# Performance work log

Measured on AMD Instinct MI355X. Metric: run time of the kernel, lower is better.

## Reference

```python
import jax, jax.numpy as jnp
import numpy as np

B, K, D = 16384, 64, 128


def setup_inputs() -> dict:
    key = jax.random.key(0)
    kx, kc = jax.random.split(key)
    x = jax.random.normal(kx, (B, D), dtype=jnp.float32)
    centers = jax.random.uniform(kc, (K, D), dtype=jnp.float32)  # torch.rand init
    return {"x": x, "centers": centers}


def reference(x, centers):
    batch, dim = x.shape
    k = centers.shape[0]
    # pairwise squared distances, same math as sum((x - c)^2)
    diff = x[:, None, :] - centers[None, :, :]          # [B, K, D]
    dist_sq = jnp.sum(diff * diff, axis=-1)             # [B, K]
    expo = -0.5 * dist_sq
    # safe softmax over clusters (identical to max-subtracted exp/sum)
    resp = jax.nn.softmax(expo, axis=-1)                # [B, K]
    log_resp = jnp.log(jnp.clip(resp, 1e-8))
    # hard assignment and per-cluster statistics
    assign = jnp.argmin(dist_sq, axis=-1)               # [B] int
    onehot = jax.nn.one_hot(assign, k, dtype=x.dtype)   # [B, K]
    cluster_weight = jnp.sum(onehot, axis=0)            # [K]
    emp_total = jnp.einsum('nk,nd->kd', onehot, x)      # [K, D]
    emp_mean = emp_total / (cluster_weight[:, None] + 1e-7)
    # masked centered samples: onehot[n,k]*(x_n - mean_k) is nonzero only at k=assign(n)
    xm = x - emp_mean[assign]                           # [B, D]
    covar_total = jnp.einsum('nk,nd,ne->kde', onehot, xm, xm)  # [K, D, D]
    covar = covar_total / (cluster_weight[:, None, None] + 1e-7)
    eye = jnp.eye(dim, dtype=x.dtype)
    covar_diag = covar * eye
    covar_off = covar * (1.0 - eye)
    diag_dist_sq = jnp.sum((covar_diag - eye) ** 2, axis=(1, 2))  # [K]
    off_dist_sq = jnp.sum(covar_off ** 2, axis=(1, 2))            # [K]
    mean_dist_sq = jnp.sum((emp_mean - centers) ** 2, axis=1)     # [K]
    mean_mse = jnp.sum(cluster_weight * mean_dist_sq) / (batch * dim)
    covar_mse = jnp.sum(
        cluster_weight * diag_dist_sq / (batch * dim)
        + cluster_weight * off_dist_sq / (batch * dim * (dim - 1.0))
    )
    return log_resp, mean_mse, covar_mse
```

## Files before the change

### kernel.cpp

```cpp
#include <hip/hip_runtime.h>

#define BB 16384
#define KK 64
#define DD 128
#define SEG 128
#define MAXITEMS 256
#define RSLAB 2048

typedef __attribute__((ext_vector_type(8))) short bf16x8;
typedef __attribute__((ext_vector_type(4))) float f32x4;

__device__ __forceinline__ unsigned int packbf2(float a, float b) {
    unsigned ua = __float_as_uint(a);
    unsigned ub = __float_as_uint(b);
    ua = (ua + 0x7FFFu + ((ua >> 16) & 1u)) >> 16;
    ub = (ub + 0x7FFFu + ((ub >> 16) & 1u)) >> 16;
    return ua | (ub << 16);
}

__global__ __launch_bounds__(256) void k_rows(
    const float* __restrict__ x, const float* __restrict__ centers,
    float* __restrict__ log_resp, int* __restrict__ assign,
    int* __restrict__ bhist, float* __restrict__ outscalars,
    float* __restrict__ emp)
{
    __shared__ float xs[64][132];
    __shared__ float ct[DD][66];
    __shared__ float cn2[KK];
    __shared__ int   lh[KK];

    const int tid = threadIdx.x;
    const int row0 = blockIdx.x * 64;

    if (blockIdx.x == 0 && tid < 2) outscalars[tid] = 0.f;
    if (tid < 32) emp[blockIdx.x * 32 + tid] = 0.f;
    if (tid < KK) lh[tid] = 0;

    for (int g = tid; g < 64 * 32; g += 256) {
        int r = g >> 5, c4 = g & 31;
        float4 v = ((const float4*)(x + (size_t)(row0 + r) * DD))[c4];
        *(float4*)&xs[r][c4 * 4] = v;
    }
    for (int g = tid; g < KK * 32; g += 256) {
        int k = g >> 5, c4 = g & 31;
        float4 v = ((const float4*)(centers + (size_t)k * DD))[c4];
        ct[c4 * 4 + 0][k] = v.x;
        ct[c4 * 4 + 1][k] = v.y;
        ct[c4 * 4 + 2][k] = v.z;
        ct[c4 * 4 + 3][k] = v.w;
    }
    __syncthreads();
    if (tid < KK) {
        float s = 0.f;
        for (int d = 0; d < DD; ++d) { float c = ct[d][tid]; s = fmaf(c, c, s); }
        cn2[tid] = s;
    }
    __syncthreads();

    const int tr = tid >> 5;
    const int tc = tid & 31;
    const int k0 = tc * 2, k1 = k0 + 1;

    float acc0[8], acc1[8];
    #pragma unroll
    for (int i = 0; i < 8; ++i) { acc0[i] = 0.f; acc1[i] = 0.f; }

    for (int d = 0; d < DD; d += 4) {
        float2 b0 = *(const float2*)&ct[d + 0][k0];
        float2 b1 = *(const float2*)&ct[d + 1][k0];
        float2 b2 = *(const float2*)&ct[d + 2][k0];
        float2 b3 = *(const float2*)&ct[d + 3][k0];
        #pragma unroll
        for (int i = 0; i < 8; ++i) {
            float4 a = *(const float4*)&xs[tr * 8 + i][d];
            acc0[i] = fmaf(a.x, b0.x, acc0[i]);
            acc1[i] = fmaf(a.x, b0.y, acc1[i]);
            acc0[i] = fmaf(a.y, b1.x, acc0[i]);
            acc1[i] = fmaf(a.y, b1.y, acc1[i]);
            acc0[i] = fmaf(a.z, b2.x, acc0[i]);
            acc1[i] = fmaf(a.z, b2.y, acc1[i]);
            acc0[i] = fmaf(a.w, b3.x, acc0[i]);
            acc1[i] = fmaf(a.w, b3.y, acc1[i]);
        }
    }

    const float cn0 = 0.5f * cn2[k0], cn1 = 0.5f * cn2[k1];
    #pragma unroll
    for (int i = 0; i < 8; ++i) {
        int row = row0 + tr * 8 + i;
        float v0 = acc0[i] - cn0;
        float v1 = acc1[i] - cn1;
        float m; int idx;
        if (v1 > v0) { m = v1; idx = k1; } else { m = v0; idx = k0; }
        #pragma unroll
        for (int off = 1; off < 32; off <<= 1) {
            float ov = __shfl_xor(m, off);
            int   oi = __shfl_xor(idx, off);
            if (ov > m || (ov == m && oi < idx)) { m = ov; idx = oi; }
        }
        float s = expf(v0 - m) + expf(v1 - m);
        #pragma unroll
        for (int off = 1; off < 32; off <<= 1) s += __shfl_xor(s, off);
        float ls = logf(s);
        float lr0 = fmaxf(v0 - m - ls, -18.4206807f);
        float lr1 = fmaxf(v1 - m - ls, -18.4206807f);
        *(float2*)&log_resp[(size_t)row * KK + k0] = make_float2(lr0, lr1);
        if (tc == 0) {
            assign[row] = idx;
            atomicAdd(&lh[idx], 1);
        }
    }
    __syncthreads();
    if (tid < KK) bhist[blockIdx.x * KK + tid] = lh[tid];
}

__global__ __launch_bounds__(256) void k_scat(
    const int* __restrict__ assign, const int* __restrict__ bhist,
    int* __restrict__ sorted, float* __restrict__ cw,
    int4* __restrict__ items, int* __restrict__ item_count,
    int* __restrict__ ist, int* __restrict__ ien)
{
    __shared__ int ph_tot[4][KK], ph_pre[4][KK];
    __shared__ int cnt_s[KK], pre_s[KK], base_s[KK], cur_s[KK];

    const int tid = threadIdx.x;
    const int b = blockIdx.x;
    const int t = tid & 63, q = tid >> 6;

    int tot = 0, pre = 0;
    const int bb0 = q * 64;
    for (int bb = bb0; bb < bb0 + 64; ++bb) {
        int v = bhist[bb * KK + t];
        tot += v;
        if (bb < b) pre += v;
    }
    ph_tot[q][t] = tot; ph_pre[q][t] = pre;
    __syncthreads();

    if (tid < KK) {
        cnt_s[tid] = ph_tot[0][tid] + ph_tot[1][tid] + ph_tot[2][tid] + ph_tot[3][tid];
        pre_s[tid] = ph_pre[0][tid] + ph_pre[1][tid] + ph_pre[2][tid] + ph_pre[3][tid];
        cur_s[tid] = 0;
    }
    __syncthreads();
    if (tid == 0) {
        int base = 0;
        for (int k = 0; k < KK; ++k) { base_s[k] = base; base += cnt_s[k]; }
    }
    __syncthreads();

    if (tid < 64) {
        int r = b * 64 + tid;
        int a = assign[r];
        int p = base_s[a] + pre_s[a] + atomicAdd(&cur_s[a], 1);
        sorted[p] = r;
    }

    if (b == 0) {
        if (tid < KK) cw[tid] = (float)cnt_s[tid];
        if (tid == 0) {
            int ic = 0;
            for (int k = 0; k < KK; ++k) {
                ist[k] = ic;
                int c = cnt_s[k];
                for (int s = 0; s < c; s += SEG) {
                    int4 it; it.x = k; it.y = base_s[k] + s;
                    it.z = min(SEG, c - s); it.w = 0;
                    items[ic++] = it;
                }
                ien[k] = ic;
            }
            *item_count = ic;
        }
    }
}

__global__ __launch_bounds__(256) void k_seg(
    const float* __restrict__ x, const int* __restrict__ sorted,
    const int4* __restrict__ items, const int* __restrict__ item_count,
    float* __restrict__ part, float* __restrict__ emp)
{
    if ((int)blockIdx.x >= *item_count) return;
    int4 it = items[blockIdx.x];
    const int k = it.x, gstart = it.y, len = it.z;

    __shared__ int rows_s[SEG];
    __shared__ unsigned int XT[DD][68];

    const int tid = threadIdx.x;
    const int w = tid >> 6, lane = tid & 63;

    if (tid < len) rows_s[tid] = sorted[gstart + tid];
    __syncthreads();

    {
        const int r0 = 2 * lane, r1 = 2 * lane + 1;
        const int d0 = w * 32;
        const float* p0 = x + (size_t)rows_s[r0 < len ? r0 : 0] * DD + d0;
        const float* p1 = x + (size_t)rows_s[r1 < len ? r1 : 0] * DD + d0;
        #pragma unroll
        for (int i = 0; i < 8; ++i) {
            float4 a = make_float4(0.f, 0.f, 0.f, 0.f);
            float4 b = make_float4(0.f, 0.f, 0.f, 0.f);
            if (r0 < len) a = *(const float4*)(p0 + 4 * i);
            if (r1 < len) b = *(const float4*)(p1 + 4 * i);
            XT[d0 + 4 * i + 0][lane] = packbf2(a.x, b.x);
            XT[d0 + 4 * i + 1][lane] = packbf2(a.y, b.y);
            XT[d0 + 4 * i + 2][lane] = packbf2(a.z, b.z);
            XT[d0 + 4 * i + 3][lane] = packbf2(a.w, b.w);
        }
    }
    __syncthreads();

    if (tid < DD) {
        float s = 0.f;
        #pragma unroll
        for (int j4 = 0; j4 < 16; ++j4) {
            uint4 v = *(const uint4*)&XT[tid][j4 * 4];
            s += __uint_as_float(v.x << 16) + __uint_as_float(v.x & 0xFFFF0000u);
            s += __uint_as_float(v.y << 16) + __uint_as_float(v.y & 0xFFFF0000u);
            s += __uint_as_float(v.z << 16) + __uint_as_float(v.z & 0xFFFF0000u);
            s += __uint_as_float(v.w << 16) + __uint_as_float(v.w & 0xFFFF0000u);
        }
        atomicAdd(&emp[k * DD + tid], s);
    }

    const int c4 = lane & 15, q = lane >> 4;
    f32x4 acc[2][8];
    #pragma unroll
    for (int h = 0; h < 2; ++h)
        #pragma unroll
        for (int nt = 0; nt < 8; ++nt)
            acc[h][nt] = (f32x4){0.f, 0.f, 0.f, 0.f};

    #pragma unroll
    for (int c = 0; c < 4; ++c) {
        const int ku = c * 16 + q * 4;
        bf16x8 a0 = *(const bf16x8*)&XT[(2 * w + 0) * 16 + c4][ku];
        bf16x8 a1 = *(const bf16x8*)&XT[(2 * w + 1) * 16 + c4][ku];
        #pragma unroll
        for (int nt = 0; nt < 8; ++nt) {
            bf16x8 b = *(const bf16x8*)&XT[nt * 16 + c4][ku];
            acc[0][nt] = __builtin_amdgcn_mfma_f32_16x16x32_bf16(a0, b, acc[0][nt], 0, 0, 0);
            acc[1][nt] = __builtin_amdgcn_mfma_f32_16x16x32_bf16(a1, b, acc[1][nt], 0, 0, 0);
        }
    }

    float* pb = part + (size_t)blockIdx.x * (DD * DD);
    #pragma unroll
    for (int h = 0; h < 2; ++h) {
        const int m0 = (2 * w + h) * 16 + q * 4;
        #pragma unroll
        for (int nt = 0; nt < 8; ++nt) {
            const int n = nt * 16 + c4;
            pb[(m0 + 0) * DD + n] = acc[h][nt].x;
            pb[(m0 + 1) * DD + n] = acc[h][nt].y;
            pb[(m0 + 2) * DD + n] = acc[h][nt].z;
            pb[(m0 + 3) * DD + n] = acc[h][nt].w;
        }
    }
}

__global__ __launch_bounds__(256) void k_redfinal(
    const float* __restrict__ part, const float* __restrict__ emp,
    const float* __restrict__ cw, const float* __restrict__ centers,
    const int* __restrict__ ist, const int* __restrict__ ien,
    float* __restrict__ outscalars)
{
    const int k = blockIdx.x >> 3;
    const int p = blockIdx.x & 7;
    const int i0 = ist[k], i1 = ien[k];
    const int tid = threadIdx.x;
    const int w = tid >> 6, lane = tid & 63;
    const float wgt = cw[k];
    const float inv = 1.0f / (wgt + 1e-7f);

    __shared__ float mu_s[DD], emp_s[DD];
    __shared__ float red[4][RSLAB];

    if (tid < DD) {
        float e = emp[k * DD + tid];
        emp_s[tid] = e;
        mu_s[tid] = e * inv;
    }

    float4 acc[8];
    #pragma unroll
    for (int c = 0; c < 8; ++c) acc[c] = make_float4(0.f, 0.f, 0.f, 0.f);

    const int base = p * RSLAB;
    for (int it = i0 + w; it < i1; it += 4) {
        const float* pb = part + (size_t)it * (DD * DD) + base;
        #pragma unroll
        for (int c = 0; c < 8; ++c) {
            float4 v = *(const float4*)&pb[c * 256 + lane * 4];
            acc[c].x += v.x; acc[c].y += v.y; acc[c].z += v.z; acc[c].w += v.w;
        }
    }
    #pragma unroll
    for (int c = 0; c < 8; ++c)
        *(float4*)&red[w][c * 256 + lane * 4] = acc[c];
    __syncthreads();

    float ds = 0.f, os = 0.f, mm = 0.f;
    #pragma unroll
    for (int jj = 0; jj < 8; ++jj) {
        int el = jj * 256 + tid;
        float sx = red[0][el] + red[1][el] + red[2][el] + red[3][el];
        int gel = base + el;
        int d = gel >> 7, e = gel & 127;
        float ctv = sx - mu_s[d] * emp_s[e] - emp_s[d] * mu_s[e]
                  + wgt * mu_s[d] * mu_s[e];
        float v = ctv * inv;
        if (d == e) { float t = v - 1.f; ds += t * t; }
        else        { os += v * v; }
    }
    if (p == 0 && tid < DD) {
        float t = mu_s[tid] - centers[k * DD + tid];
        mm = t * t;
    }

    #pragma unroll
    for (int off = 32; off > 0; off >>= 1) {
        ds += __shfl_down(ds, off);
        os += __shfl_down(os, off);
        mm += __shfl_down(mm, off);
    }
    __shared__ float rds[4], ros[4], rmm[4];
    if (lane == 0) { rds[w] = ds; ros[w] = os; rmm[w] = mm; }
    __syncthreads();
    if (tid == 0) {
        float DS = rds[0] + rds[1] + rds[2] + rds[3];
        float OS = ros[0] + ros[1] + ros[2] + ros[3];
        float MM = rmm[0] + rmm[1] + rmm[2] + rmm[3];
        const float bd = (float)BB * (float)DD;
        atomicAdd(&outscalars[0], wgt * MM / bd);
        atomicAdd(&outscalars[1], wgt * DS / bd + wgt * OS / (bd * (float)(DD - 1)));
    }
}

extern "C" void kernel_launch(void* const* d_in, const int* in_sizes, int n_in,
                              void* d_out, int out_size, void* d_ws, size_t ws_size,
                              hipStream_t stream) {
    const float* x = (const float*)d_in[0];
    const float* centers = (const float*)d_in[1];
    float* out = (float*)d_out;
    float* outscalars = out + (size_t)BB * KK;

    char* ws = (char*)d_ws;
    size_t off = 0;
    float* part    = (float*)(ws + off); off += (size_t)MAXITEMS * DD * DD * 4;
    float* emp     = (float*)(ws + off); off += KK * DD * 4;
    int*   sorted  = (int*)  (ws + off); off += BB * 4;
    int*   assign  = (int*)  (ws + off); off += BB * 4;
    int*   bhist   = (int*)  (ws + off); off += 256 * KK * 4;
    int4*  items   = (int4*) (ws + off); off += MAXITEMS * 16;
    float* cw      = (float*)(ws + off); off += 256;
    int*   itemcnt = (int*)  (ws + off); off += 256;
    int*   ist     = (int*)  (ws + off); off += 256;
    int*   ien     = (int*)  (ws + off); off += 256;

    k_rows    <<<256, 256, 0, stream>>>(x, centers, out, assign, bhist,
                                        outscalars, emp);
    k_scat    <<<256, 256, 0, stream>>>(assign, bhist, sorted, cw, items,
                                        itemcnt, ist, ien);
    k_seg     <<<MAXITEMS, 256, 0, stream>>>(x, sorted, items, itemcnt, part, emp);
    k_redfinal<<<KK * 8, 256, 0, stream>>>(part, emp, cw, centers, ist, ien,
                                           outscalars);
}
```

Measured before the change: 128.3 us.

## Double segment length per block and spread partial reduction across more blocks

Each k_seg block now handles up to 256 rows of its cluster in two 128-row halves, keeping MFMA accumulators in registers across both halves. That halves the number of 128x128 partial covariance slabs written to and re-read from global memory. The final reduction now uses 64 blocks per cluster with one element per thread and no shared-memory staging, giving more parallelism. k_seg launches only 128 blocks, so there is less parallelism there, and the halves run serially within each block.

```diff
diff --git a/kernel.cpp b/kernel.cpp
--- a/kernel.cpp
+++ b/kernel.cpp
@@ -3,9 +3,9 @@
 #define BB 16384
 #define KK 64
 #define DD 128
-#define SEG 128
+#define SEG 256
 #define MAXITEMS 256
-#define RSLAB 2048
+#define NS 64
 
 typedef __attribute__((ext_vector_type(8))) short bf16x8;
 typedef __attribute__((ext_vector_type(4))) float f32x4;
@@ -184,67 +184,77 @@
     int4 it = items[blockIdx.x];
     const int k = it.x, gstart = it.y, len = it.z;
 
-    __shared__ int rows_s[SEG];
+    __shared__ int rows_s[128];
     __shared__ unsigned int XT[DD][68];
 
     const int tid = threadIdx.x;
     const int w = tid >> 6, lane = tid & 63;
-
-    if (tid < len) rows_s[tid] = sorted[gstart + tid];
-    __syncthreads();
-
-    {
-        const int r0 = 2 * lane, r1 = 2 * lane + 1;
-        const int d0 = w * 32;
-        const float* p0 = x + (size_t)rows_s[r0 < len ? r0 : 0] * DD + d0;
-        const float* p1 = x + (size_t)rows_s[r1 < len ? r1 : 0] * DD + d0;
-        #pragma unroll
-        for (int i = 0; i < 8; ++i) {
-            float4 a = make_float4(0.f, 0.f, 0.f, 0.f);
-            float4 b = make_float4(0.f, 0.f, 0.f, 0.f);
-            if (r0 < len) a = *(const float4*)(p0 + 4 * i);
-            if (r1 < len) b = *(const float4*)(p1 + 4 * i);
-            XT[d0 + 4 * i + 0][lane] = packbf2(a.x, b.x);
-            XT[d0 + 4 * i + 1][lane] = packbf2(a.y, b.y);
-            XT[d0 + 4 * i + 2][lane] = packbf2(a.z, b.z);
-            XT[d0 + 4 * i + 3][lane] = packbf2(a.w, b.w);
-        }
-    }
-    __syncthreads();
-
-    if (tid < DD) {
-        float s = 0.f;
-        #pragma unroll
-        for (int j4 = 0; j4 < 16; ++j4) {
-            uint4 v = *(const uint4*)&XT[tid][j4 * 4];
-            s += __uint_as_float(v.x << 16) + __uint_as_float(v.x & 0xFFFF0000u);
-            s += __uint_as_float(v.y << 16) + __uint_as_float(v.y & 0xFFFF0000u);
-            s += __uint_as_float(v.z << 16) + __uint_as_float(v.z & 0xFFFF0000u);
-            s += __uint_as_float(v.w << 16) + __uint_as_float(v.w & 0xFFFF0000u);
-        }
-        atomicAdd(&emp[k * DD + tid], s);
-    }
-
     const int c4 = lane & 15, q = lane >> 4;
+
     f32x4 acc[2][8];
     #pragma unroll
     for (int h = 0; h < 2; ++h)
         #pragma unroll
         for (int nt = 0; nt < 8; ++nt)
             acc[h][nt] = (f32x4){0.f, 0.f, 0.f, 0.f};
-
-    #pragma unroll
-    for (int c = 0; c < 4; ++c) {
-        const int ku = c * 16 + q * 4;
-        bf16x8 a0 = *(const bf16x8*)&XT[(2 * w + 0) * 16 + c4][ku];
-        bf16x8 a1 = *(const bf16x8*)&XT[(2 * w + 1) * 16 + c4][ku];
-        #pragma unroll
-        for (int nt = 0; nt < 8; ++nt) {
-            bf16x8 b = *(const bf16x8*)&XT[nt * 16 + c4][ku];
-            acc[0][nt] = __builtin_amdgcn_mfma_f32_16x16x32_bf16(a0, b, acc[0][nt], 0, 0, 0);
-            acc[1][nt] = __builtin_amdgcn_mfma_f32_16x16x32_bf16(a1, b, acc[1][nt], 0, 0, 0);
-        }
-    }
+    float colsum = 0.f;
+
+    for (int half = 0; half < 2; ++half) {
+        const int hoff = half * 128;
+        const int hlen = min(128, len - hoff);
+        if (hlen <= 0) break;
+
+        __syncthreads();
+        if (tid < hlen) rows_s[tid] = sorted[gstart + hoff + tid];
+        __syncthreads();
+
+        {
+            const int r0 = 2 * lane, r1 = 2 * lane + 1;
+            const int d0 = w * 32;
+            const float* p0 = x + (size_t)rows_s[r0 < hlen ? r0 : 0] * DD + d0;
+            const float* p1 = x + (size_t)rows_s[r1 < hlen ? r1 : 0] * DD + d0;
+            #pragma unroll
+            for (int i = 0; i < 8; ++i) {
+                float4 a = make_float4(0.f, 0.f, 0.f, 0.f);
+                float4 b = make_float4(0.f, 0.f, 0.f, 0.f);
+                if (r0 < hlen) a = *(const float4*)(p0 + 4 * i);
+                if (r1 < hlen) b = *(const float4*)(p1 + 4 * i);
+                XT[d0 + 4 * i + 0][lane] = packbf2(a.x, b.x);
+                XT[d0 + 4 * i + 1][lane] = packbf2(a.y, b.y);
+                XT[d0 + 4 * i + 2][lane] = packbf2(a.z, b.z);
+                XT[d0 + 4 * i + 3][lane] = packbf2(a.w, b.w);
+            }
+        }
+        __syncthreads();
+
+        if (tid < DD) {
+            float s = 0.f;
+            #pragma unroll
+            for (int j4 = 0; j4 < 16; ++j4) {
+                uint4 v = *(const uint4*)&XT[tid][j4 * 4];
+                s += __uint_as_float(v.x << 16) + __uint_as_float(v.x & 0xFFFF0000u);
+                s += __uint_as_float(v.y << 16) + __uint_as_float(v.y & 0xFFFF0000u);
+                s += __uint_as_float(v.z << 16) + __uint_as_float(v.z & 0xFFFF0000u);
+                s += __uint_as_float(v.w << 16) + __uint_as_float(v.w & 0xFFFF0000u);
+            }
+            colsum += s;
+        }
+
+        #pragma unroll
+        for (int c = 0; c < 4; ++c) {
+            const int ku = c * 16 + q * 4;
+            bf16x8 a0 = *(const bf16x8*)&XT[(2 * w + 0) * 16 + c4][ku];
+            bf16x8 a1 = *(const bf16x8*)&XT[(2 * w + 1) * 16 + c4][ku];
+            #pragma unroll
+            for (int nt = 0; nt < 8; ++nt) {
+                bf16x8 b = *(const bf16x8*)&XT[nt * 16 + c4][ku];
+                acc[0][nt] = __builtin_amdgcn_mfma_f32_16x16x32_bf16(a0, b, acc[0][nt], 0, 0, 0);
+                acc[1][nt] = __builtin_amdgcn_mfma_f32_16x16x32_bf16(a1, b, acc[1][nt], 0, 0, 0);
+            }
+        }
+    }
+
+    if (tid < DD) atomicAdd(&emp[k * DD + tid], colsum);
 
     float* pb = part + (size_t)blockIdx.x * (DD * DD);
     #pragma unroll
@@ -267,8 +277,8 @@
     const int* __restrict__ ist, const int* __restrict__ ien,
     float* __restrict__ outscalars)
 {
-    const int k = blockIdx.x >> 3;
-    const int p = blockIdx.x & 7;
+    const int k = blockIdx.x >> 6;
+    const int p = blockIdx.x & (NS - 1);
     const int i0 = ist[k], i1 = ien[k];
     const int tid = threadIdx.x;
     const int w = tid >> 6, lane = tid & 63;
@@ -276,45 +286,30 @@
     const float inv = 1.0f / (wgt + 1e-7f);
 
     __shared__ float mu_s[DD], emp_s[DD];
-    __shared__ float red[4][RSLAB];
-
     if (tid < DD) {
         float e = emp[k * DD + tid];
         emp_s[tid] = e;
         mu_s[tid] = e * inv;
     }
-
-    float4 acc[8];
-    #pragma unroll
-    for (int c = 0; c < 8; ++c) acc[c] = make_float4(0.f, 0.f, 0.f, 0.f);
-
-    const int base = p * RSLAB;
-    for (int it = i0 + w; it < i1; it += 4) {
-        const float* pb = part + (size_t)it * (DD * DD) + base;
-        #pragma unroll
-        for (int c = 0; c < 8; ++c) {
-            float4 v = *(const float4*)&pb[c * 256 + lane * 4];
-            acc[c].x += v.x; acc[c].y += v.y; acc[c].z += v.z; acc[c].w += v.w;
-        }
-    }
-    #pragma unroll
-    for (int c = 0; c < 8; ++c)
-        *(float4*)&red[w][c * 256 + lane * 4] = acc[c];
-    __syncthreads();
-
+    __syncthreads();
+
+    const int gel = p * 256 + tid;
+    float s0 = 0.f, s1 = 0.f;
+    int it = i0;
+    for (; it + 1 < i1; it += 2) {
+        s0 += part[(size_t)it * (DD * DD) + gel];
+        s1 += part[(size_t)(it + 1) * (DD * DD) + gel];
+    }
+    if (it < i1) s0 += part[(size_t)it * (DD * DD) + gel];
+    const float sx = s0 + s1;
+
+    const int d = gel >> 7, e = gel & 127;
+    float ctv = sx - mu_s[d] * emp_s[e] - emp_s[d] * mu_s[e]
+              + wgt * mu_s[d] * mu_s[e];
+    float v = ctv * inv;
     float ds = 0.f, os = 0.f, mm = 0.f;
-    #pragma unroll
-    for (int jj = 0; jj < 8; ++jj) {
-        int el = jj * 256 + tid;
-        float sx = red[0][el] + red[1][el] + red[2][el] + red[3][el];
-        int gel = base + el;
-        int d = gel >> 7, e = gel & 127;
-        float ctv = sx - mu_s[d] * emp_s[e] - emp_s[d] * mu_s[e]
-                  + wgt * mu_s[d] * mu_s[e];
-        float v = ctv * inv;
-        if (d == e) { float t = v - 1.f; ds += t * t; }
-        else        { os += v * v; }
-    }
+    if (d == e) { float t = v - 1.f; ds = t * t; }
+    else        { os = v * v; }
     if (p == 0 && tid < DD) {
         float t = mu_s[tid] - centers[k * DD + tid];
         mm = t * t;
@@ -364,7 +359,7 @@
                                         outscalars, emp);
     k_scat    <<<256, 256, 0, stream>>>(assign, bhist, sorted, cw, items,
                                         itemcnt, ist, ien);
-    k_seg     <<<MAXITEMS, 256, 0, stream>>>(x, sorted, items, itemcnt, part, emp);
-    k_redfinal<<<KK * 8, 256, 0, stream>>>(part, emp, cw, centers, ist, ien,
-                                           outscalars);
-}
+    k_seg     <<<128, 256, 0, stream>>>(x, sorted, items, itemcnt, part, emp);
+    k_redfinal<<<KK * NS, 256, 0, stream>>>(part, emp, cw, centers, ist, ien,
+                                            outscalars);
+}
```

After: 220.4 us. 71.7% more time.

## Double segment length, replace atomics with per-item partials and last-block reduce

Applied to the files above, without the earlier changes.

Each k_seg block now handles up to 256 rows in two 128-row halves and accumulates into the same MFMA registers. That halves the number of 128x128 partial covariance matrices written to and re-read from global memory. The per-cluster column-sum atomics are replaced by per-item partial vectors, which k_redfinal sums itself. The final scalar atomics become a counter-based last-block reduction over per-block results. In exchange, k_redfinal uses a 64 KB shared slab per block, which lowers occupancy, and k_seg has more serial work per block.

```diff
diff --git a/kernel.cpp b/kernel.cpp
--- a/kernel.cpp
+++ b/kernel.cpp
@@ -3,9 +3,11 @@
 #define BB 16384
 #define KK 64
 #define DD 128
-#define SEG 128
-#define MAXITEMS 256
-#define RSLAB 2048
+#define SEG 256
+#define MAXITEMS 128
+#define NRB 4
+#define RSLAB 4096
+#define RBLKS (KK * NRB)
 
 typedef __attribute__((ext_vector_type(8))) short bf16x8;
 typedef __attribute__((ext_vector_type(4))) float f32x4;
@@ -21,8 +23,7 @@
 __global__ __launch_bounds__(256) void k_rows(
     const float* __restrict__ x, const float* __restrict__ centers,
     float* __restrict__ log_resp, int* __restrict__ assign,
-    int* __restrict__ bhist, float* __restrict__ outscalars,
-    float* __restrict__ emp)
+    int* __restrict__ bhist, int* __restrict__ counter)
 {
     __shared__ float xs[64][132];
     __shared__ float ct[DD][66];
@@ -32,8 +33,7 @@
     const int tid = threadIdx.x;
     const int row0 = blockIdx.x * 64;
 
-    if (blockIdx.x == 0 && tid < 2) outscalars[tid] = 0.f;
-    if (tid < 32) emp[blockIdx.x * 32 + tid] = 0.f;
+    if (blockIdx.x == 0 && tid == 0) *counter = 0;
     if (tid < KK) lh[tid] = 0;
 
     for (int g = tid; g < 64 * 32; g += 256) {
@@ -178,73 +178,83 @@
 __global__ __launch_bounds__(256) void k_seg(
     const float* __restrict__ x, const int* __restrict__ sorted,
     const int4* __restrict__ items, const int* __restrict__ item_count,
-    float* __restrict__ part, float* __restrict__ emp)
+    float* __restrict__ part, float* __restrict__ emp_part)
 {
     if ((int)blockIdx.x >= *item_count) return;
     int4 it = items[blockIdx.x];
-    const int k = it.x, gstart = it.y, len = it.z;
-
-    __shared__ int rows_s[SEG];
+    const int gstart = it.y, len = it.z;
+
+    __shared__ int rows_s[128];
     __shared__ unsigned int XT[DD][68];
 
     const int tid = threadIdx.x;
     const int w = tid >> 6, lane = tid & 63;
-
-    if (tid < len) rows_s[tid] = sorted[gstart + tid];
-    __syncthreads();
-
-    {
-        const int r0 = 2 * lane, r1 = 2 * lane + 1;
-        const int d0 = w * 32;
-        const float* p0 = x + (size_t)rows_s[r0 < len ? r0 : 0] * DD + d0;
-        const float* p1 = x + (size_t)rows_s[r1 < len ? r1 : 0] * DD + d0;
-        #pragma unroll
-        for (int i = 0; i < 8; ++i) {
-            float4 a = make_float4(0.f, 0.f, 0.f, 0.f);
-            float4 b = make_float4(0.f, 0.f, 0.f, 0.f);
-            if (r0 < len) a = *(const float4*)(p0 + 4 * i);
-            if (r1 < len) b = *(const float4*)(p1 + 4 * i);
-            XT[d0 + 4 * i + 0][lane] = packbf2(a.x, b.x);
-            XT[d0 + 4 * i + 1][lane] = packbf2(a.y, b.y);
-            XT[d0 + 4 * i + 2][lane] = packbf2(a.z, b.z);
-            XT[d0 + 4 * i + 3][lane] = packbf2(a.w, b.w);
-        }
-    }
-    __syncthreads();
-
-    if (tid < DD) {
-        float s = 0.f;
-        #pragma unroll
-        for (int j4 = 0; j4 < 16; ++j4) {
-            uint4 v = *(const uint4*)&XT[tid][j4 * 4];
-            s += __uint_as_float(v.x << 16) + __uint_as_float(v.x & 0xFFFF0000u);
-            s += __uint_as_float(v.y << 16) + __uint_as_float(v.y & 0xFFFF0000u);
-            s += __uint_as_float(v.z << 16) + __uint_as_float(v.z & 0xFFFF0000u);
-            s += __uint_as_float(v.w << 16) + __uint_as_float(v.w & 0xFFFF0000u);
-        }
-        atomicAdd(&emp[k * DD + tid], s);
-    }
-
     const int c4 = lane & 15, q = lane >> 4;
+
     f32x4 acc[2][8];
     #pragma unroll
     for (int h = 0; h < 2; ++h)
         #pragma unroll
         for (int nt = 0; nt < 8; ++nt)
             acc[h][nt] = (f32x4){0.f, 0.f, 0.f, 0.f};
-
-    #pragma unroll
-    for (int c = 0; c < 4; ++c) {
-        const int ku = c * 16 + q * 4;
-        bf16x8 a0 = *(const bf16x8*)&XT[(2 * w + 0) * 16 + c4][ku];
-        bf16x8 a1 = *(const bf16x8*)&XT[(2 * w + 1) * 16 + c4][ku];
-        #pragma unroll
-        for (int nt = 0; nt < 8; ++nt) {
-            bf16x8 b = *(const bf16x8*)&XT[nt * 16 + c4][ku];
-            acc[0][nt] = __builtin_amdgcn_mfma_f32_16x16x32_bf16(a0, b, acc[0][nt], 0, 0, 0);
-            acc[1][nt] = __builtin_amdgcn_mfma_f32_16x16x32_bf16(a1, b, acc[1][nt], 0, 0, 0);
-        }
-    }
+    float colsum = 0.f;
+
+    for (int half = 0; half < 2; ++half) {
+        const int hoff = half * 128;
+        const int hlen = min(128, len - hoff);
+        if (hlen <= 0) break;
+
+        __syncthreads();
+        if (tid < hlen) rows_s[tid] = sorted[gstart + hoff + tid];
+        __syncthreads();
+
+        {
+            const int r0 = 2 * lane, r1 = 2 * lane + 1;
+            const int d0 = w * 32;
+            const float* p0 = x + (size_t)rows_s[r0 < hlen ? r0 : 0] * DD + d0;
+            const float* p1 = x + (size_t)rows_s[r1 < hlen ? r1 : 0] * DD + d0;
+            #pragma unroll
+            for (int i = 0; i < 8; ++i) {
+                float4 a = make_float4(0.f, 0.f, 0.f, 0.f);
+                float4 b = make_float4(0.f, 0.f, 0.f, 0.f);
+                if (r0 < hlen) a = *(const float4*)(p0 + 4 * i);
+                if (r1 < hlen) b = *(const float4*)(p1 + 4 * i);
+                XT[d0 + 4 * i + 0][lane] = packbf2(a.x, b.x);
+                XT[d0 + 4 * i + 1][lane] = packbf2(a.y, b.y);
+                XT[d0 + 4 * i + 2][lane] = packbf2(a.z, b.z);
+                XT[d0 + 4 * i + 3][lane] = packbf2(a.w, b.w);
+            }
+        }
+        __syncthreads();
+
+        if (tid < DD) {
+            float s = 0.f;
+            #pragma unroll
+            for (int j4 = 0; j4 < 16; ++j4) {
+                uint4 v = *(const uint4*)&XT[tid][j4 * 4];
+                s += __uint_as_float(v.x << 16) + __uint_as_float(v.x & 0xFFFF0000u);
+                s += __uint_as_float(v.y << 16) + __uint_as_float(v.y & 0xFFFF0000u);
+                s += __uint_as_float(v.z << 16) + __uint_as_float(v.z & 0xFFFF0000u);
+                s += __uint_as_float(v.w << 16) + __uint_as_float(v.w & 0xFFFF0000u);
+            }
+            colsum += s;
+        }
+
+        #pragma unroll
+        for (int c = 0; c < 4; ++c) {
+            const int ku = c * 16 + q * 4;
+            bf16x8 a0 = *(const bf16x8*)&XT[(2 * w + 0) * 16 + c4][ku];
+            bf16x8 a1 = *(const bf16x8*)&XT[(2 * w + 1) * 16 + c4][ku];
+            #pragma unroll
+            for (int nt = 0; nt < 8; ++nt) {
+                bf16x8 b = *(const bf16x8*)&XT[nt * 16 + c4][ku];
+                acc[0][nt] = __builtin_amdgcn_mfma_f32_16x16x32_bf16(a0, b, acc[0][nt], 0, 0, 0);
+                acc[1][nt] = __builtin_amdgcn_mfma_f32_16x16x32_bf16(a1, b, acc[1][nt], 0, 0, 0);
+            }
+        }
+    }
+
+    if (tid < DD) emp_part[blockIdx.x * DD + tid] = colsum;
 
     float* pb = part + (size_t)blockIdx.x * (DD * DD);
     #pragma unroll
@@ -262,13 +272,14 @@
 }
 
 __global__ __launch_bounds__(256) void k_redfinal(
-    const float* __restrict__ part, const float* __restrict__ emp,
+    const float* __restrict__ part, const float* __restrict__ emp_part,
     const float* __restrict__ cw, const float* __restrict__ centers,
     const int* __restrict__ ist, const int* __restrict__ ien,
+    float2* __restrict__ spart, int* __restrict__ counter,
     float* __restrict__ outscalars)
 {
-    const int k = blockIdx.x >> 3;
-    const int p = blockIdx.x & 7;
+    const int k = blockIdx.x >> 2;
+    const int p = blockIdx.x & 3;
     const int i0 = ist[k], i1 = ien[k];
     const int tid = threadIdx.x;
     const int w = tid >> 6, lane = tid & 63;
@@ -276,35 +287,48 @@
     const float inv = 1.0f / (wgt + 1e-7f);
 
     __shared__ float mu_s[DD], emp_s[DD];
+    __shared__ float emp2[2][DD];
     __shared__ float red[4][RSLAB];
 
+    {
+        const int dh = tid & 127, hf = tid >> 7;
+        float e0 = 0.f, e1 = 0.f;
+        int it = i0 + hf;
+        for (; it + 2 < i1; it += 4) {
+            e0 += emp_part[it * DD + dh];
+            e1 += emp_part[(it + 2) * DD + dh];
+        }
+        if (it < i1) e0 += emp_part[it * DD + dh];
+        emp2[hf][dh] = e0 + e1;
+    }
+    __syncthreads();
     if (tid < DD) {
-        float e = emp[k * DD + tid];
+        float e = emp2[0][tid] + emp2[1][tid];
         emp_s[tid] = e;
         mu_s[tid] = e * inv;
     }
 
-    float4 acc[8];
-    #pragma unroll
-    for (int c = 0; c < 8; ++c) acc[c] = make_float4(0.f, 0.f, 0.f, 0.f);
+    float4 acc[16];
+    #pragma unroll
+    for (int c = 0; c < 16; ++c) acc[c] = make_float4(0.f, 0.f, 0.f, 0.f);
 
     const int base = p * RSLAB;
     for (int it = i0 + w; it < i1; it += 4) {
         const float* pb = part + (size_t)it * (DD * DD) + base;
         #pragma unroll
-        for (int c = 0; c < 8; ++c) {
+        for (int c = 0; c < 16; ++c) {
             float4 v = *(const float4*)&pb[c * 256 + lane * 4];
             acc[c].x += v.x; acc[c].y += v.y; acc[c].z += v.z; acc[c].w += v.w;
         }
     }
     #pragma unroll
-    for (int c = 0; c < 8; ++c)
+    for (int c = 0; c < 16; ++c)
         *(float4*)&red[w][c * 256 + lane * 4] = acc[c];
     __syncthreads();
 
     float ds = 0.f, os = 0.f, mm = 0.f;
     #pragma unroll
-    for (int jj = 0; jj < 8; ++jj) {
+    for (int jj = 0; jj < 16; ++jj) {
         int el = jj * 256 + tid;
         float sx = red[0][el] + red[1][el] + red[2][el] + red[3][el];
         int gel = base + el;
@@ -327,6 +351,7 @@
         mm += __shfl_down(mm, off);
     }
     __shared__ float rds[4], ros[4], rmm[4];
+    __shared__ int is_last;
     if (lane == 0) { rds[w] = ds; ros[w] = os; rmm[w] = mm; }
     __syncthreads();
     if (tid == 0) {
@@ -334,8 +359,31 @@
         float OS = ros[0] + ros[1] + ros[2] + ros[3];
         float MM = rmm[0] + rmm[1] + rmm[2] + rmm[3];
         const float bd = (float)BB * (float)DD;
-        atomicAdd(&outscalars[0], wgt * MM / bd);
-        atomicAdd(&outscalars[1], wgt * DS / bd + wgt * OS / (bd * (float)(DD - 1)));
+        float2 mine;
+        mine.x = wgt * MM / bd;
+        mine.y = wgt * DS / bd + wgt * OS / (bd * (float)(DD - 1));
+        spart[blockIdx.x] = mine;
+        __threadfence();
+        int old = atomicAdd(counter, 1);
+        is_last = (old == RBLKS - 1);
+    }
+    __syncthreads();
+    if (is_last) {
+        __threadfence();
+        float2 v = (tid < RBLKS) ? spart[tid] : make_float2(0.f, 0.f);
+        float a = v.x, b = v.y;
+        #pragma unroll
+        for (int off = 32; off > 0; off >>= 1) {
+            a += __shfl_down(a, off);
+            b += __shfl_down(b, off);
+        }
+        __shared__ float ra[4], rb[4];
+        if (lane == 0) { ra[w] = a; rb[w] = b; }
+        __syncthreads();
+        if (tid == 0) {
+            outscalars[0] = ra[0] + ra[1] + ra[2] + ra[3];
+            outscalars[1] = rb[0] + rb[1] + rb[2] + rb[3];
+        }
     }
 }
 
@@ -349,22 +397,24 @@
 
     char* ws = (char*)d_ws;
     size_t off = 0;
-    float* part    = (float*)(ws + off); off += (size_t)MAXITEMS * DD * DD * 4;
-    float* emp     = (float*)(ws + off); off += KK * DD * 4;
-    int*   sorted  = (int*)  (ws + off); off += BB * 4;
-    int*   assign  = (int*)  (ws + off); off += BB * 4;
-    int*   bhist   = (int*)  (ws + off); off += 256 * KK * 4;
-    int4*  items   = (int4*) (ws + off); off += MAXITEMS * 16;
-    float* cw      = (float*)(ws + off); off += 256;
-    int*   itemcnt = (int*)  (ws + off); off += 256;
-    int*   ist     = (int*)  (ws + off); off += 256;
-    int*   ien     = (int*)  (ws + off); off += 256;
-
-    k_rows    <<<256, 256, 0, stream>>>(x, centers, out, assign, bhist,
-                                        outscalars, emp);
+    float*  part     = (float*)(ws + off); off += (size_t)MAXITEMS * DD * DD * 4;
+    float*  emp_part = (float*)(ws + off); off += MAXITEMS * DD * 4;
+    int*    sorted   = (int*)  (ws + off); off += BB * 4;
+    int*    assign   = (int*)  (ws + off); off += BB * 4;
+    int*    bhist    = (int*)  (ws + off); off += 256 * KK * 4;
+    int4*   items    = (int4*) (ws + off); off += 256 * 16;
+    float*  cw       = (float*)(ws + off); off += 256;
+    int*    itemcnt  = (int*)  (ws + off); off += 256;
+    int*    ist      = (int*)  (ws + off); off += 256;
+    int*    ien      = (int*)  (ws + off); off += 256;
+    float2* spart    = (float2*)(ws + off); off += RBLKS * 8;
+    int*    counter  = (int*)  (ws + off); off += 256;
+
+    k_rows    <<<256, 256, 0, stream>>>(x, centers, out, assign, bhist, counter);
     k_scat    <<<256, 256, 0, stream>>>(assign, bhist, sorted, cw, items,
                                         itemcnt, ist, ien);
-    k_seg     <<<MAXITEMS, 256, 0, stream>>>(x, sorted, items, itemcnt, part, emp);
-    k_redfinal<<<KK * 8, 256, 0, stream>>>(part, emp, cw, centers, ist, ien,
-                                           outscalars);
-}
+    k_seg     <<<MAXITEMS, 256, 0, stream>>>(x, sorted, items, itemcnt,
+                                             part, emp_part);
+    k_redfinal<<<RBLKS, 256, 0, stream>>>(part, emp_part, cw, centers, ist, ien,
+                                          spart, counter, outscalars);
+}
```

Measured after the change: 126.5 us. No clear change (-1.5%).
